# Optimization experiments

Measured on AMD Instinct MI355X. Metric: run time of the kernel, lower is better.

## Reference

```python
import jax, jax.numpy as jnp
import numpy as np

XSIZE = 128
B = 8
N = 262144


def setup_inputs() -> dict:
    key = jax.random.key(0)
    k1, k2 = jax.random.split(key)
    indices = jax.random.randint(k1, (B, N, 3), 0, XSIZE, dtype=jnp.int32)
    values = jax.random.normal(k2, (B, N), dtype=jnp.float32)
    return {"indices": indices, "values": values, "xsize": XSIZE}


def reference(indices, values, xsize):
    # Batched equivalent of tf.map_fn(tensor_scatter_nd_add) per sample:
    # scatter-add N point values into a zero (xsize, xsize, xsize) grid.
    def build_grid(idx, val):
        grid = jnp.zeros((xsize, xsize, xsize), dtype=val.dtype)
        return grid.at[idx[:, 0], idx[:, 1], idx[:, 2]].add(val)

    grid = jax.vmap(build_grid)(indices, values)  # [B, X, X, X]

    # Adjacent-voxel differences along each spatial axis
    d1 = grid[:, 1:, :, :] - grid[:, :-1, :, :]
    d2 = grid[:, :, 1:, :] - grid[:, :, :-1, :]
    d3 = grid[:, :, :, 1:] - grid[:, :, :, :-1]

    ax = (1, 2, 3)
    # Total variation loss: sum |diff| / num_voxels (xsize^3)
    num_voxels = jnp.float32(xsize * xsize * xsize)
    tv = (jnp.sum(jnp.abs(d1), axis=ax)
          + jnp.sum(jnp.abs(d2), axis=ax)
          + jnp.sum(jnp.abs(d3), axis=ax)) / num_voxels

    # MSE smoothness loss: sum diff^2 / (2*xsize^2 - 2*xsize)
    # (faithful to TF code, which uses only shape[1:3] for the denominator)
    num_pairs = jnp.float32(2 * xsize * xsize - 2 * xsize)
    mse = (jnp.sum(jnp.square(d1), axis=ax)
           + jnp.sum(jnp.square(d2), axis=ax)
           + jnp.sum(jnp.square(d3), axis=ax)) / num_pairs

    return tv, mse
```

## Files before the change

kernel.cpp:

```cpp
#include <hip/hip_runtime.h>
#include <hip/hip_fp16.h>

constexpr unsigned XS        = 128;
constexpr unsigned NB        = 8;
constexpr unsigned NPTS      = 262144;
constexpr unsigned TOTAL_PTS = NB * NPTS;
constexpr unsigned PPB       = 4096;
constexpr unsigned NSEG      = TOTAL_PTS / PPB;
constexpr unsigned NBKT      = NB * XS;
constexpr unsigned CAP       = 3072;

constexpr size_t REC2_U32 = (size_t)NBKT * CAP;

__global__ __launch_bounds__(512) void bin_kernel(
        const int* __restrict__ idx, const float* __restrict__ vals,
        unsigned* __restrict__ rec2, unsigned* __restrict__ gcur) {
    __shared__ unsigned long long sbuf[PPB];
    __shared__ unsigned hist[XS], cur[XS], loff[XS], gbase[XS];
    unsigned tid = threadIdx.x, g = blockIdx.x;
    unsigned b = g >> 6;
    unsigned base = g * PPB;

    if (tid < XS) hist[tid] = 0u;

    unsigned key[8]; float val[8];
    const unsigned* ibuf = (const unsigned*)sbuf;
    for (unsigned r = 0; r < 2u; ++r) {
        __syncthreads();
        {
            const uint4* src = (const uint4*)idx + ((size_t)g * 3072u + r * 1536u);
            uint4* dst = (uint4*)sbuf;
#pragma unroll
            for (unsigned n = 0; n < 3u; ++n) dst[n * 512u + tid] = src[n * 512u + tid];
        }
        __syncthreads();
#pragma unroll
        for (unsigned n = 0; n < 4u; ++n) {
            unsigned p = n * 512u + tid;
            unsigned i = ibuf[3u * p], j = ibuf[3u * p + 1u], k = ibuf[3u * p + 2u];
            unsigned m = r * 4u + n;
            key[m] = (i << 14) | (j << 7) | k;
            val[m] = vals[base + r * 2048u + p];
            atomicAdd(&hist[i], 1u);
        }
    }
    __syncthreads();

    if (tid < 64u) {
        unsigned h0 = hist[tid], h1 = hist[64u + tid];
        unsigned a0 = h0, a1 = h1;
#pragma unroll
        for (unsigned o = 1; o <= 32; o <<= 1) {
            unsigned t0 = __shfl_up(a0, o, 64);
            unsigned t1 = __shfl_up(a1, o, 64);
            if (tid >= o) { a0 += t0; a1 += t1; }
        }
        a1 += __shfl(a0, 63, 64);
        unsigned e0 = a0 - h0, e1 = a1 - h1;
        loff[tid] = e0; loff[64u + tid] = e1;
        cur[tid]  = e0; cur[64u + tid]  = e1;
    }
    __syncthreads();
    if (tid < XS) gbase[tid] = atomicAdd(&gcur[b * XS + tid], hist[tid]);

#pragma unroll
    for (unsigned m = 0; m < 8u; ++m) {
        unsigned i = key[m] >> 14;
        unsigned pos = atomicAdd(&cur[i], 1u);
        sbuf[pos] = ((unsigned long long)__float_as_uint(val[m]) << 32)
                  | (unsigned long long)key[m];
    }
    __syncthreads();

#pragma unroll
    for (unsigned m = 0; m < 8u; ++m) {
        unsigned s = m * 512u + tid;
        unsigned long long rr = sbuf[s];
        unsigned bin = ((unsigned)rr >> 14) & 127u;
        unsigned dst = gbase[bin] + (s - loff[bin]);
        unsigned short hv = __half_as_ushort(
            __float2half(__uint_as_float((unsigned)(rr >> 32))));
        if (dst < CAP)
            __builtin_nontemporal_store(
                ((unsigned)hv << 16) | ((unsigned)rr & 0x3FFFu),
                &rec2[(size_t)(b * XS + bin) * CAP + dst]);
    }
}

__global__ __launch_bounds__(512) void accum_kernel(
        const unsigned* __restrict__ rec2,
        const unsigned* __restrict__ gcur, float* __restrict__ stage) {
    __shared__ float strip[65u * XS];
    __shared__ float sred[16];
    unsigned z = blockIdx.x;
    unsigned b = z >> 7, i = z & 127u;
    bool has_d1 = (i < 127u);
    unsigned tid = threadIdx.x, lane = tid & 63u, w = tid >> 6;

    unsigned cnt0 = min(gcur[b * XS + i], CAP);
    unsigned cnt1 = has_d1 ? min(gcur[b * XS + i + 1u], CAP) : 0u;
    const unsigned long long* bA =
        (const unsigned long long*)(rec2 + (size_t)(b * XS + i) * CAP);
    const unsigned long long* bB =
        (const unsigned long long*)(rec2 + (size_t)(b * XS + i + 1u) * CAP);

    unsigned long long rvA[3]; bool avA[3];
    unsigned long long rvB[3]; bool avB[3];
#pragma unroll
    for (unsigned q = 0; q < 3u; ++q) {
        unsigned r2 = q * 512u + tid;
        avA[q] = (2u * r2) < cnt0;
        if (avA[q]) rvA[q] = __builtin_nontemporal_load(bA + r2);
    }
#pragma unroll
    for (unsigned q = 0; q < 3u; ++q) {
        unsigned r2 = q * 512u + tid;
        avB[q] = has_d1 && (2u * r2) < cnt1;
        if (avB[q]) rvB[q] = __builtin_nontemporal_load(bB + r2);
    }

    float tvb = 0.f, mseb = 0.f;
    for (unsigned t = 0; t < 2u; ++t) {
        unsigned j0 = t << 6;
        auto process = [&](unsigned rc, float sg, unsigned lmax) {
            unsigned l = ((rc >> 7) & 127u) - j0;
            if (l <= lmax)
                atomicAdd(&strip[(l << 7) | (rc & 127u)],
                          sg * __half2float(__ushort_as_half((unsigned short)(rc >> 16))));
        };

        __syncthreads();
        float4* p4 = (float4*)strip;
        for (unsigned r = tid; r < 2080u; r += 512u)
            p4[r] = float4{0.f, 0.f, 0.f, 0.f};
        __syncthreads();

#pragma unroll
        for (unsigned q = 0; q < 3u; ++q)
            if (avA[q]) {
                unsigned r0 = 2u * (q * 512u + tid);
                process((unsigned)rvA[q], 1.f, 64u);
                if (r0 + 1u < cnt0) process((unsigned)(rvA[q] >> 32), 1.f, 64u);
            }
        __syncthreads();

        unsigned jmax = 127u - j0;
        float tv = 0.f, mse = 0.f;
#pragma unroll
        for (unsigned r = 0; r < 4u; ++r) {
            unsigned v4 = r * 512u + tid;
            unsigned l = v4 >> 5, k4 = v4 & 31u;
            float4 c = p4[v4];
            float d0 = c.y - c.x, d1 = c.z - c.y, d2 = c.w - c.z;
            tv  += fabsf(d0) + fabsf(d1) + fabsf(d2);
            mse += d0 * d0 + d1 * d1 + d2 * d2;
            if (k4 < 31u) {
                float nx = strip[(v4 << 2) + 4u];
                float d3 = nx - c.w;
                tv += fabsf(d3); mse += d3 * d3;
            }
            if (l < jmax) {
                float4 n = p4[v4 + 32u];
                float e0 = n.x - c.x, e1 = n.y - c.y, e2 = n.z - c.z, e3 = n.w - c.w;
                tv  += fabsf(e0) + fabsf(e1) + fabsf(e2) + fabsf(e3);
                mse += e0 * e0 + e1 * e1 + e2 * e2 + e3 * e3;
            }
        }

        if (has_d1) {
            __syncthreads();
#pragma unroll
            for (unsigned q = 0; q < 3u; ++q)
                if (avB[q]) {
                    unsigned r0 = 2u * (q * 512u + tid);
                    process((unsigned)rvB[q], -1.f, 63u);
                    if (r0 + 1u < cnt1) process((unsigned)(rvB[q] >> 32), -1.f, 63u);
                }
            __syncthreads();
#pragma unroll
            for (unsigned r = 0; r < 4u; ++r) {
                float4 dd = p4[r * 512u + tid];
                tv  += fabsf(dd.x) + fabsf(dd.y) + fabsf(dd.z) + fabsf(dd.w);
                mse += dd.x * dd.x + dd.y * dd.y + dd.z * dd.z + dd.w * dd.w;
            }
        }
        tvb += tv; mseb += mse;
    }

#pragma unroll
    for (int o = 32; o > 0; o >>= 1) {
        tvb  += __shfl_down(tvb, o, 64);
        mseb += __shfl_down(mseb, o, 64);
    }
    if (lane == 0u) { sred[w] = tvb; sred[8u + w] = mseb; }
    __syncthreads();
    if (tid == 0u) {
        float tt = 0.f, mm = 0.f;
#pragma unroll
        for (unsigned q = 0; q < 8u; ++q) { tt += sred[q]; mm += sred[8u + q]; }
        atomicAdd(stage + (size_t)b * 16u,        tt);
        atomicAdd(stage + (size_t)(8u + b) * 16u, mm);
    }
}

__global__ void finalize_kernel(const float* __restrict__ stage,
                                float* __restrict__ out) {
    unsigned i = threadIdx.x;
    if (i < 16u) {
        float s = stage[i * 16u];
        float scale = (i < 8u) ? (1.0f / 2097152.0f)
                               : (1.0f / 32512.0f);
        out[i] = s * scale;
    }
}

extern "C" void kernel_launch(void* const* d_in, const int* in_sizes, int n_in,
                              void* d_out, int out_size, void* d_ws, size_t ws_size,
                              hipStream_t stream) {
    const int*   idx  = (const int*)d_in[0];
    const float* vals = (const float*)d_in[1];

    unsigned* rec2  = (unsigned*)d_ws;
    unsigned* gcur  = rec2 + REC2_U32;
    float*    stage = (float*)(gcur + NBKT);
    float*    out   = (float*)d_out;

    hipMemsetAsync(gcur, 0, NBKT * 4 + 256 * 4, stream);

    bin_kernel<<<NSEG, 512, 0, stream>>>(idx, vals, rec2, gcur);
    accum_kernel<<<NBKT, 512, 0, stream>>>(rec2, gcur, stage);
    finalize_kernel<<<1, 64, 0, stream>>>(stage, out);
}
```

Before: 115.5 us.

## Split slabs into half-slab bins with halo duplication and fuse finalize into accum

The binning now keys each point by x-slab and y-half, giving 256 bins per batch, and duplicates points at j==64 into the lower half-bin as a halo. Each accum block then handles one half-slab in a single pass instead of two sequential passes over a full slab, which doubles the block count and shortens per-block work. Bin blocks shrink to 2048 points, index and value loads become nontemporal, and the separate finalize launch is replaced by a last-block-done counter inside accum. The costs are extra duplicated records, more global atomics on the bin counters, and a threadfence-plus-atomic completion handshake.

```diff
diff --git a/kernel.cpp b/kernel.cpp
--- a/kernel.cpp
+++ b/kernel.cpp
@@ -5,194 +5,212 @@
 constexpr unsigned NB        = 8;
 constexpr unsigned NPTS      = 262144;
 constexpr unsigned TOTAL_PTS = NB * NPTS;
-constexpr unsigned PPB       = 4096;
+constexpr unsigned PPB       = 2048;
 constexpr unsigned NSEG      = TOTAL_PTS / PPB;
-constexpr unsigned NBKT      = NB * XS;
-constexpr unsigned CAP       = 3072;
-
-constexpr size_t REC2_U32 = (size_t)NBKT * CAP;
+constexpr unsigned NBIN      = 256;
+constexpr unsigned NBKT      = NB * NBIN;
+constexpr unsigned CAP       = 1536;
+constexpr size_t   REC2_U32  = (size_t)NBKT * CAP;
+
+typedef unsigned int u32x4 __attribute__((ext_vector_type(4)));
+
 
 __global__ __launch_bounds__(512) void bin_kernel(
         const int* __restrict__ idx, const float* __restrict__ vals,
         unsigned* __restrict__ rec2, unsigned* __restrict__ gcur) {
-    __shared__ unsigned long long sbuf[PPB];
-    __shared__ unsigned hist[XS], cur[XS], loff[XS], gbase[XS];
+    __shared__ u32x4 stage4[1536];
+    __shared__ unsigned hist[NBIN], cur[NBIN], loff[NBIN], gbase[NBIN];
+    __shared__ unsigned stot;
+    unsigned long long* sbuf = (unsigned long long*)stage4;
+
     unsigned tid = threadIdx.x, g = blockIdx.x;
-    unsigned b = g >> 6;
+    unsigned b = g >> 7;
     unsigned base = g * PPB;
 
-    if (tid < XS) hist[tid] = 0u;
-
-    unsigned key[8]; float val[8];
-    const unsigned* ibuf = (const unsigned*)sbuf;
-    for (unsigned r = 0; r < 2u; ++r) {
-        __syncthreads();
-        {
-            const uint4* src = (const uint4*)idx + ((size_t)g * 3072u + r * 1536u);
-            uint4* dst = (uint4*)sbuf;
-#pragma unroll
-            for (unsigned n = 0; n < 3u; ++n) dst[n * 512u + tid] = src[n * 512u + tid];
-        }
-        __syncthreads();
-#pragma unroll
-        for (unsigned n = 0; n < 4u; ++n) {
-            unsigned p = n * 512u + tid;
-            unsigned i = ibuf[3u * p], j = ibuf[3u * p + 1u], k = ibuf[3u * p + 2u];
-            unsigned m = r * 4u + n;
-            key[m] = (i << 14) | (j << 7) | k;
-            val[m] = vals[base + r * 2048u + p];
-            atomicAdd(&hist[i], 1u);
-        }
+    if (tid < NBIN) hist[tid] = 0u;
+
+    {
+        const u32x4* src = (const u32x4*)idx + (size_t)g * 1536u;
+#pragma unroll
+        for (unsigned n = 0; n < 3u; ++n)
+            stage4[n * 512u + tid] = __builtin_nontemporal_load(src + n * 512u + tid);
+    }
+    __syncthreads();
+
+    const unsigned* ibuf = (const unsigned*)stage4;
+    unsigned low[4]; float val[4]; bool dup[4];
+#pragma unroll
+    for (unsigned n = 0; n < 4u; ++n) {
+        unsigned p = n * 512u + tid;
+        unsigned i = ibuf[3u * p], j = ibuf[3u * p + 1u], k = ibuf[3u * p + 2u];
+        val[n] = __builtin_nontemporal_load(vals + base + p);
+        unsigned bin = (i << 1) | (j >> 6);
+        low[n] = (bin << 21) | (i << 14) | (j << 7) | k;
+        atomicAdd(&hist[bin], 1u);
+        dup[n] = (j == 64u);
+        if (dup[n]) atomicAdd(&hist[i << 1], 1u);
     }
     __syncthreads();
 
     if (tid < 64u) {
-        unsigned h0 = hist[tid], h1 = hist[64u + tid];
-        unsigned a0 = h0, a1 = h1;
+        unsigned h0 = hist[tid],        h1 = hist[64u + tid],
+                 h2 = hist[128u + tid], h3 = hist[192u + tid];
+        unsigned a0 = h0, a1 = h1, a2 = h2, a3 = h3;
 #pragma unroll
         for (unsigned o = 1; o <= 32; o <<= 1) {
-            unsigned t0 = __shfl_up(a0, o, 64);
-            unsigned t1 = __shfl_up(a1, o, 64);
-            if (tid >= o) { a0 += t0; a1 += t1; }
+            unsigned t0 = __shfl_up(a0, o, 64), t1 = __shfl_up(a1, o, 64);
+            unsigned t2 = __shfl_up(a2, o, 64), t3 = __shfl_up(a3, o, 64);
+            if (tid >= o) { a0 += t0; a1 += t1; a2 += t2; a3 += t3; }
         }
         a1 += __shfl(a0, 63, 64);
-        unsigned e0 = a0 - h0, e1 = a1 - h1;
-        loff[tid] = e0; loff[64u + tid] = e1;
-        cur[tid]  = e0; cur[64u + tid]  = e1;
-    }
-    __syncthreads();
-    if (tid < XS) gbase[tid] = atomicAdd(&gcur[b * XS + tid], hist[tid]);
-
-#pragma unroll
-    for (unsigned m = 0; m < 8u; ++m) {
-        unsigned i = key[m] >> 14;
-        unsigned pos = atomicAdd(&cur[i], 1u);
-        sbuf[pos] = ((unsigned long long)__float_as_uint(val[m]) << 32)
-                  | (unsigned long long)key[m];
-    }
-    __syncthreads();
-
-#pragma unroll
-    for (unsigned m = 0; m < 8u; ++m) {
-        unsigned s = m * 512u + tid;
+        a2 += __shfl(a1, 63, 64);
+        a3 += __shfl(a2, 63, 64);
+        loff[tid] = a0 - h0; loff[64u + tid] = a1 - h1;
+        loff[128u + tid] = a2 - h2; loff[192u + tid] = a3 - h3;
+        cur[tid] = a0 - h0; cur[64u + tid] = a1 - h1;
+        cur[128u + tid] = a2 - h2; cur[192u + tid] = a3 - h3;
+        if (tid == 63u) stot = a3;
+    }
+    __syncthreads();
+    if (tid < NBIN) gbase[tid] = atomicAdd(&gcur[b * NBIN + tid], hist[tid]);
+
+#pragma unroll
+    for (unsigned n = 0; n < 4u; ++n) {
+        unsigned bin = low[n] >> 21;
+        unsigned long long r = ((unsigned long long)__float_as_uint(val[n]) << 32)
+                             | (unsigned long long)low[n];
+        sbuf[atomicAdd(&cur[bin], 1u)] = r;
+        if (dup[n])
+            sbuf[atomicAdd(&cur[bin - 1u], 1u)] = r - 0x200000ull;
+    }
+    __syncthreads();
+
+    unsigned tot = stot;
+    for (unsigned s = tid; s < tot; s += 512u) {
         unsigned long long rr = sbuf[s];
-        unsigned bin = ((unsigned)rr >> 14) & 127u;
+        unsigned lo = (unsigned)rr;
+        unsigned bin = lo >> 21;
         unsigned dst = gbase[bin] + (s - loff[bin]);
         unsigned short hv = __half_as_ushort(
             __float2half(__uint_as_float((unsigned)(rr >> 32))));
         if (dst < CAP)
             __builtin_nontemporal_store(
-                ((unsigned)hv << 16) | ((unsigned)rr & 0x3FFFu),
-                &rec2[(size_t)(b * XS + bin) * CAP + dst]);
+                ((unsigned)hv << 16) | (lo & 0x3FFFu),
+                &rec2[(size_t)(b * NBIN + bin) * CAP + dst]);
     }
 }
 
 __global__ __launch_bounds__(512) void accum_kernel(
-        const unsigned* __restrict__ rec2,
-        const unsigned* __restrict__ gcur, float* __restrict__ stage) {
+        const unsigned* __restrict__ rec2, const unsigned* __restrict__ gcur,
+        float* __restrict__ stage, float* __restrict__ out,
+        unsigned* __restrict__ done) {
     __shared__ float strip[65u * XS];
     __shared__ float sred[16];
     unsigned z = blockIdx.x;
-    unsigned b = z >> 7, i = z & 127u;
+    unsigned b = z >> 8, r = z & 255u, i = r >> 1, h = r & 1u;
+    unsigned tid = threadIdx.x, lane = tid & 63u, w = tid >> 6;
     bool has_d1 = (i < 127u);
-    unsigned tid = threadIdx.x, lane = tid & 63u, w = tid >> 6;
-
-    unsigned cnt0 = min(gcur[b * XS + i], CAP);
-    unsigned cnt1 = has_d1 ? min(gcur[b * XS + i + 1u], CAP) : 0u;
+
+    unsigned cnt0 = min(gcur[b * NBIN + r], CAP);
+    unsigned cnt1 = has_d1 ? min(gcur[b * NBIN + r + 2u], CAP) : 0u;
     const unsigned long long* bA =
-        (const unsigned long long*)(rec2 + (size_t)(b * XS + i) * CAP);
+        (const unsigned long long*)(rec2 + (size_t)(b * NBIN + r) * CAP);
     const unsigned long long* bB =
-        (const unsigned long long*)(rec2 + (size_t)(b * XS + i + 1u) * CAP);
-
-    unsigned long long rvA[3]; bool avA[3];
-    unsigned long long rvB[3]; bool avB[3];
-#pragma unroll
-    for (unsigned q = 0; q < 3u; ++q) {
+        (const unsigned long long*)(rec2 + (size_t)(b * NBIN + r + 2u) * CAP);
+
+    unsigned long long rvA[2], rvB[2]; bool avA[2], avB[2];
+#pragma unroll
+    for (unsigned q = 0; q < 2u; ++q) {
         unsigned r2 = q * 512u + tid;
-        avA[q] = (2u * r2) < cnt0;
+        avA[q] = (r2 < 768u) && (2u * r2 < cnt0);
         if (avA[q]) rvA[q] = __builtin_nontemporal_load(bA + r2);
-    }
-#pragma unroll
-    for (unsigned q = 0; q < 3u; ++q) {
-        unsigned r2 = q * 512u + tid;
-        avB[q] = has_d1 && (2u * r2) < cnt1;
+        avB[q] = (r2 < 768u) && (2u * r2 < cnt1);
         if (avB[q]) rvB[q] = __builtin_nontemporal_load(bB + r2);
     }
 
-    float tvb = 0.f, mseb = 0.f;
-    for (unsigned t = 0; t < 2u; ++t) {
-        unsigned j0 = t << 6;
-        auto process = [&](unsigned rc, float sg, unsigned lmax) {
-            unsigned l = ((rc >> 7) & 127u) - j0;
-            if (l <= lmax)
+    float4* p4 = (float4*)strip;
+    for (unsigned v = tid; v < 2080u; v += 512u) p4[v] = float4{0.f, 0.f, 0.f, 0.f};
+    __syncthreads();
+
+    unsigned j0 = h << 6;
+#pragma unroll
+    for (unsigned q = 0; q < 2u; ++q)
+        if (avA[q]) {
+            unsigned r0 = 2u * (q * 512u + tid);
+            {
+                unsigned rc = (unsigned)rvA[q];
+                unsigned l = ((rc >> 7) & 127u) - j0;
                 atomicAdd(&strip[(l << 7) | (rc & 127u)],
-                          sg * __half2float(__ushort_as_half((unsigned short)(rc >> 16))));
-        };
-
+                          __half2float(__ushort_as_half((unsigned short)(rc >> 16))));
+            }
+            if (r0 + 1u < cnt0) {
+                unsigned rc = (unsigned)(rvA[q] >> 32);
+                unsigned l = ((rc >> 7) & 127u) - j0;
+                atomicAdd(&strip[(l << 7) | (rc & 127u)],
+                          __half2float(__ushort_as_half((unsigned short)(rc >> 16))));
+            }
+        }
+    __syncthreads();
+
+    unsigned jpmax = 64u - h;
+    float tv = 0.f, mse = 0.f;
+#pragma unroll
+    for (unsigned n = 0; n < 4u; ++n) {
+        unsigned v4 = n * 512u + tid;
+        unsigned l = v4 >> 5, k4 = v4 & 31u;
+        float4 c = p4[v4];
+        float d0 = c.y - c.x, d1v = c.z - c.y, d2v = c.w - c.z;
+        tv  += fabsf(d0) + fabsf(d1v) + fabsf(d2v);
+        mse += d0 * d0 + d1v * d1v + d2v * d2v;
+        if (k4 < 31u) {
+            float nx = strip[(v4 << 2) + 4u];
+            float d3 = nx - c.w;
+            tv += fabsf(d3); mse += d3 * d3;
+        }
+        if (l < jpmax) {
+            float4 nr = p4[v4 + 32u];
+            float e0 = nr.x - c.x, e1 = nr.y - c.y, e2 = nr.z - c.z, e3 = nr.w - c.w;
+            tv  += fabsf(e0) + fabsf(e1) + fabsf(e2) + fabsf(e3);
+            mse += e0 * e0 + e1 * e1 + e2 * e2 + e3 * e3;
+        }
+    }
+
+    if (has_d1) {
         __syncthreads();
-        float4* p4 = (float4*)strip;
-        for (unsigned r = tid; r < 2080u; r += 512u)
-            p4[r] = float4{0.f, 0.f, 0.f, 0.f};
+#pragma unroll
+        for (unsigned q = 0; q < 2u; ++q)
+            if (avB[q]) {
+                unsigned r0 = 2u * (q * 512u + tid);
+                {
+                    unsigned rc = (unsigned)rvB[q];
+                    unsigned l = ((rc >> 7) & 127u) - j0;
+                    if (l < 64u)
+                        atomicAdd(&strip[(l << 7) | (rc & 127u)],
+                                  -__half2float(__ushort_as_half((unsigned short)(rc >> 16))));
+                }
+                if (r0 + 1u < cnt1) {
+                    unsigned rc = (unsigned)(rvB[q] >> 32);
+                    unsigned l = ((rc >> 7) & 127u) - j0;
+                    if (l < 64u)
+                        atomicAdd(&strip[(l << 7) | (rc & 127u)],
+                                  -__half2float(__ushort_as_half((unsigned short)(rc >> 16))));
+                }
+            }
         __syncthreads();
-
-#pragma unroll
-        for (unsigned q = 0; q < 3u; ++q)
-            if (avA[q]) {
-                unsigned r0 = 2u * (q * 512u + tid);
-                process((unsigned)rvA[q], 1.f, 64u);
-                if (r0 + 1u < cnt0) process((unsigned)(rvA[q] >> 32), 1.f, 64u);
-            }
-        __syncthreads();
-
-        unsigned jmax = 127u - j0;
-        float tv = 0.f, mse = 0.f;
-#pragma unroll
-        for (unsigned r = 0; r < 4u; ++r) {
-            unsigned v4 = r * 512u + tid;
-            unsigned l = v4 >> 5, k4 = v4 & 31u;
-            float4 c = p4[v4];
-            float d0 = c.y - c.x, d1 = c.z - c.y, d2 = c.w - c.z;
-            tv  += fabsf(d0) + fabsf(d1) + fabsf(d2);
-            mse += d0 * d0 + d1 * d1 + d2 * d2;
-            if (k4 < 31u) {
-                float nx = strip[(v4 << 2) + 4u];
-                float d3 = nx - c.w;
-                tv += fabsf(d3); mse += d3 * d3;
-            }
-            if (l < jmax) {
-                float4 n = p4[v4 + 32u];
-                float e0 = n.x - c.x, e1 = n.y - c.y, e2 = n.z - c.z, e3 = n.w - c.w;
-                tv  += fabsf(e0) + fabsf(e1) + fabsf(e2) + fabsf(e3);
-                mse += e0 * e0 + e1 * e1 + e2 * e2 + e3 * e3;
-            }
-        }
-
-        if (has_d1) {
-            __syncthreads();
-#pragma unroll
-            for (unsigned q = 0; q < 3u; ++q)
-                if (avB[q]) {
-                    unsigned r0 = 2u * (q * 512u + tid);
-                    process((unsigned)rvB[q], -1.f, 63u);
-                    if (r0 + 1u < cnt1) process((unsigned)(rvB[q] >> 32), -1.f, 63u);
-                }
-            __syncthreads();
-#pragma unroll
-            for (unsigned r = 0; r < 4u; ++r) {
-                float4 dd = p4[r * 512u + tid];
-                tv  += fabsf(dd.x) + fabsf(dd.y) + fabsf(dd.z) + fabsf(dd.w);
-                mse += dd.x * dd.x + dd.y * dd.y + dd.z * dd.z + dd.w * dd.w;
-            }
-        }
-        tvb += tv; mseb += mse;
+#pragma unroll
+        for (unsigned n = 0; n < 4u; ++n) {
+            float4 dd = p4[n * 512u + tid];
+            tv  += fabsf(dd.x) + fabsf(dd.y) + fabsf(dd.z) + fabsf(dd.w);
+            mse += dd.x * dd.x + dd.y * dd.y + dd.z * dd.z + dd.w * dd.w;
+        }
     }
 
 #pragma unroll
     for (int o = 32; o > 0; o >>= 1) {
-        tvb  += __shfl_down(tvb, o, 64);
-        mseb += __shfl_down(mseb, o, 64);
-    }
-    if (lane == 0u) { sred[w] = tvb; sred[8u + w] = mseb; }
+        tv  += __shfl_down(tv, o, 64);
+        mse += __shfl_down(mse, o, 64);
+    }
+    if (lane == 0u) { sred[w] = tv; sred[8u + w] = mse; }
     __syncthreads();
     if (tid == 0u) {
         float tt = 0.f, mm = 0.f;
@@ -200,17 +218,17 @@
         for (unsigned q = 0; q < 8u; ++q) { tt += sred[q]; mm += sred[8u + q]; }
         atomicAdd(stage + (size_t)b * 16u,        tt);
         atomicAdd(stage + (size_t)(8u + b) * 16u, mm);
-    }
-}
-
-__global__ void finalize_kernel(const float* __restrict__ stage,
-                                float* __restrict__ out) {
-    unsigned i = threadIdx.x;
-    if (i < 16u) {
-        float s = stage[i * 16u];
-        float scale = (i < 8u) ? (1.0f / 2097152.0f)
-                               : (1.0f / 32512.0f);
-        out[i] = s * scale;
+        __threadfence();
+        unsigned t = atomicAdd(done, 1u);
+        if (t == 2047u) {
+#pragma unroll
+            for (unsigned q = 0; q < 16u; ++q) {
+                float s = atomicAdd(stage + (size_t)q * 16u, 0.0f);
+                float scale = (q < 8u) ? (1.0f / 2097152.0f)
+                                       : (1.0f / 32512.0f);
+                out[q] = s * scale;
+            }
+        }
     }
 }
 
@@ -223,11 +241,11 @@
     unsigned* rec2  = (unsigned*)d_ws;
     unsigned* gcur  = rec2 + REC2_U32;
     float*    stage = (float*)(gcur + NBKT);
+    unsigned* done  = (unsigned*)(stage + 256);
     float*    out   = (float*)d_out;
 
-    hipMemsetAsync(gcur, 0, NBKT * 4 + 256 * 4, stream);
+    (void)hipMemsetAsync(gcur, 0, NBKT * 4 + 256 * 4 + 4, stream);
 
     bin_kernel<<<NSEG, 512, 0, stream>>>(idx, vals, rec2, gcur);
-    accum_kernel<<<NBKT, 512, 0, stream>>>(rec2, gcur, stage);
-    finalize_kernel<<<1, 64, 0, stream>>>(stage, out);
+    accum_kernel<<<NBKT, 512, 0, stream>>>(rec2, gcur, stage, out, done);
 }
```

Measured after the change: 158.5 us. 37.2% more time.
